# Kernel optimization log

Measured on AMD Instinct MI355X. Metric: run time of the kernel, lower is better.

The kernel has to match this reference:

```python
import jax, jax.numpy as jnp
import numpy as np

N_NODES, HID = 100000, 128
B, C, L, K = 64, 16, 256, 4


def setup_inputs() -> dict:
    key = jax.random.key(0)
    ks = jax.random.split(key, 6)
    s = 1.0 / np.sqrt(HID)
    return {
        "x": jax.random.normal(ks[0], (N_NODES, HID), dtype=jnp.float32),
        "leaf_idx": jax.random.randint(ks[1], (B, C, L), 0, N_NODES),
        "W_z": jax.random.normal(ks[2], (K, HID, HID), dtype=jnp.float32) * s,
        "W_z_final": jax.random.normal(ks[3], (HID, HID), dtype=jnp.float32) * s,
        "W_p": jax.random.normal(ks[4], (HID, HID), dtype=jnp.float32) * s,
        "W_p_final": jax.random.normal(ks[5], (HID, HID), dtype=jnp.float32) * s,
    }


def reference(x, leaf_idx, W_z, W_z_final, W_p, W_p_final):
    # Fixed ptree per sample: {'P': [{'Z': [L leaves]} x C]}
    k = W_z.shape[0]
    data = x[leaf_idx]                                   # [B,C,L,H] leaf gather (batch.x[subtree])
    # ---- z_layer_fn (vectorized over B,C) ----
    y = jnp.einsum("bclh,koh->kbclo", data, W_z)         # k bias-free Linears
    y = jax.vmap(lambda yk, s: jnp.roll(yk, -s, axis=2))(y, jnp.arange(k))  # roll along L by -idx
    z = jax.nn.elu(y.sum(axis=0))                        # sum over k, ELU  [B,C,L,H]
    z = jnp.einsum("bclh,oh->bclo", z, W_z_final).sum(axis=2)  # final linear, sum over L
    z = jax.nn.elu(z)                                    # [B,C,H]
    # ---- p_layer_fn over the C Z-children ----
    p = jnp.einsum("bch,oh->bco", z, W_p).sum(axis=1)    # p_layer, sum over children
    # apply_p_elu=False -> identity
    out = p @ W_p_final.T                                # [B,H]
    return out
```

## Files before the change

kernel.cpp:

```cpp
#include <hip/hip_runtime.h>
#include <hip/hip_bf16.h>

#define N_NODES 100000
#define HID 128
#define BB 64
#define CC 16
#define LL 256

typedef __bf16 b16x8 __attribute__((ext_vector_type(8)));
typedef float f32x4 __attribute__((ext_vector_type(4)));

__device__ __forceinline__ unsigned int bf16pair(float a, float b) {
  unsigned int ua = __float_as_uint(a), ub = __float_as_uint(b);
  ua = (ua + 0x7FFFu + ((ua >> 16) & 1u)) >> 16;
  ub = (ub + 0x7FFFu + ((ub >> 16) & 1u)) >> 16;
  return ua | (ub << 16);
}

__device__ __forceinline__ unsigned int cvtpk(float a, float b) {
  unsigned int r;
  asm("v_cvt_pk_bf16_f32 %0, %1, %2" : "=v"(r) : "v"(a), "v"(b));
  return r;
}

__device__ __forceinline__ float elu(float v) {
  return v > 0.f ? v : (__expf(v) - 1.f);
}

__global__ void k_prep(const float* __restrict__ Wz, uint4* __restrict__ wfrag) {
  const int u = blockIdx.x * 256 + threadIdx.x;
  const int lane = u & 63;
  const int ot = (u >> 6) & 7;
  const int ks = (u >> 9) & 3;
  const int kk = u >> 11;
  const int o = ot * 16 + (lane & 15);
  const int h0 = kk * 32 + (lane >> 4) * 8;
  const float4* src = (const float4*)(Wz + ((size_t)(ks * HID + o) * HID + h0));
  float4 f0 = src[0], f1 = src[1];
  uint4 pk;
  pk.x = bf16pair(f0.x, f0.y);
  pk.y = bf16pair(f0.z, f0.w);
  pk.z = bf16pair(f1.x, f1.y);
  pk.w = bf16pair(f1.z, f1.w);
  wfrag[u] = pk;
}

__global__ __launch_bounds__(512, 4) void k_main(
    const float* __restrict__ x, const int* __restrict__ leaf_idx,
    const uint4* __restrict__ wfrag, float* __restrict__ zsum) {
  extern __shared__ char smem[];
  char* sA = smem;
  uint4* sW = (uint4*)(smem + 65536);

  const int tid = threadIdx.x;
  const int bc = blockIdx.x;
  const int lane = tid & 63;
  const int l15 = lane & 15;
  const int hi = lane >> 4;
  const int w = tid >> 6;
  const int wr = w >> 1;
  const int wc = w & 1;

  {
    const int r = tid >> 1, half = tid & 1;
    const int idx = leaf_idx[bc * LL + r];
    const float4* src = (const float4*)(x + (size_t)idx * HID + half * 64);
    const int swz = (r & 15) << 4;
    char* rowp = sA + r * 256;
#pragma unroll
    for (int j = 0; j < 8; ++j) {
      float4 f0 = src[2 * j];
      float4 f1 = src[2 * j + 1];
      uint4 pk;
      pk.x = cvtpk(f0.x, f0.y);
      pk.y = cvtpk(f0.z, f0.w);
      pk.z = cvtpk(f1.x, f1.y);
      pk.w = cvtpk(f1.z, f1.w);
      *(uint4*)(rowp + (((half * 128) + j * 16) ^ swz)) = pk;
    }
  }
  sW[tid] = wfrag[tid];
  sW[512 + tid] = wfrag[512 + tid];
  __syncthreads();

  f32x4 acc[4][4];
#pragma unroll
  for (int rt = 0; rt < 4; ++rt)
#pragma unroll
    for (int ot = 0; ot < 4; ++ot) acc[rt][ot] = (f32x4){0.f, 0.f, 0.f, 0.f};

  const int r0 = wr * 64;

#pragma unroll
  for (int c = 0; c < 16; ++c) {
    const int kk = c >> 2, ks = c & 3;
    uint4 pref;
    if (c < 14) pref = wfrag[(c + 2) * 512 + tid];

    const uint4* sWc = sW + (c & 1) * 512;
    const int cb = kk * 64 + hi * 16;
    uint4 af[4];
#pragma unroll
    for (int rt = 0; rt < 4; ++rt) {
      const int row = (r0 + rt * 16 + l15 + ks) & 255;
      af[rt] = *(const uint4*)(sA + row * 256 + (cb ^ ((row & 15) << 4)));
    }
    __builtin_amdgcn_s_setprio(1);
#pragma unroll
    for (int ot2 = 0; ot2 < 4; ++ot2) {
      const uint4 bw = sWc[(wc * 4 + ot2) * 64 + lane];
      const b16x8 bb = __builtin_bit_cast(b16x8, bw);
#pragma unroll
      for (int rt = 0; rt < 4; ++rt)
        acc[rt][ot2] = __builtin_amdgcn_mfma_f32_16x16x32_bf16(
            __builtin_bit_cast(b16x8, af[rt]), bb, acc[rt][ot2], 0, 0, 0);
    }
    __builtin_amdgcn_s_setprio(0);
    __syncthreads();
    if (c < 14) sW[(c & 1) * 512 + tid] = pref;
  }

  float colsum[4];
#pragma unroll
  for (int ot2 = 0; ot2 < 4; ++ot2) {
    float s = 0.f;
#pragma unroll
    for (int rt = 0; rt < 4; ++rt)
#pragma unroll
      for (int q = 0; q < 4; ++q) s += elu(acc[rt][ot2][q]);
    s += __shfl_xor(s, 16);
    s += __shfl_xor(s, 32);
    colsum[ot2] = s;
  }
  float* sRed = (float*)sA;
  if (lane < 16) {
#pragma unroll
    for (int ot2 = 0; ot2 < 4; ++ot2)
      sRed[w * 64 + ot2 * 16 + lane] = colsum[ot2];
  }
  __syncthreads();
  if (tid < 128) {
    const int wc2 = tid >> 6, lc = tid & 63;
    float s = 0.f;
#pragma unroll
    for (int wrr = 0; wrr < 4; ++wrr) s += sRed[(wrr * 2 + wc2) * 64 + lc];
    zsum[bc * 128 + tid] = s;
  }
}

__global__ __launch_bounds__(512) void k_tail(
    const float* __restrict__ zsum, const float* __restrict__ Wzf,
    const float* __restrict__ Wp, const float* __restrict__ Wpf,
    float* __restrict__ out) {
  __shared__ float sZ[CC * HID];
  __shared__ float sS[4][HID];
  __shared__ float sV[HID];
  __shared__ float sP[HID];
  const int tid = threadIdx.x, b = blockIdx.x;
#pragma unroll
  for (int j = 0; j < 4; ++j)
    sZ[tid + j * 512] = zsum[(size_t)b * (CC * HID) + tid + j * 512];
  __syncthreads();

  {
    const int o = tid & 127, g = tid >> 7;
    const float4* wr4 = (const float4*)(Wzf + o * HID);
    float d0 = 0.f, d1 = 0.f, d2 = 0.f, d3 = 0.f;
#pragma unroll
    for (int j = 0; j < 32; ++j) {
      const float4 wv = wr4[j];
      const float4 z0 = *(const float4*)(sZ + (g * 4 + 0) * HID + j * 4);
      const float4 z1 = *(const float4*)(sZ + (g * 4 + 1) * HID + j * 4);
      const float4 z2v = *(const float4*)(sZ + (g * 4 + 2) * HID + j * 4);
      const float4 z3 = *(const float4*)(sZ + (g * 4 + 3) * HID + j * 4);
      d0 += wv.x * z0.x + wv.y * z0.y + wv.z * z0.z + wv.w * z0.w;
      d1 += wv.x * z1.x + wv.y * z1.y + wv.z * z1.z + wv.w * z1.w;
      d2 += wv.x * z2v.x + wv.y * z2v.y + wv.z * z2v.z + wv.w * z2v.w;
      d3 += wv.x * z3.x + wv.y * z3.y + wv.z * z3.z + wv.w * z3.w;
    }
    sS[g][o] = elu(d0) + elu(d1) + elu(d2) + elu(d3);
  }
  __syncthreads();
  if (tid < HID) sV[tid] = sS[0][tid] + sS[1][tid] + sS[2][tid] + sS[3][tid];
  __syncthreads();

  {
    const int o2 = tid >> 2, sub = tid & 3;
    const float4* wp4 = (const float4*)(Wp + o2 * HID + sub * 32);
    const float4* v4 = (const float4*)(sV + sub * 32);
    float d0 = 0.f, d1 = 0.f;
#pragma unroll
    for (int j = 0; j < 8; j += 2) {
      float4 a0 = wp4[j], c0 = v4[j];
      float4 a1 = wp4[j + 1], c1 = v4[j + 1];
      d0 += a0.x * c0.x + a0.y * c0.y + a0.z * c0.z + a0.w * c0.w;
      d1 += a1.x * c1.x + a1.y * c1.y + a1.z * c1.z + a1.w * c1.w;
    }
    float d = d0 + d1;
    d += __shfl_xor(d, 1);
    d += __shfl_xor(d, 2);
    if (sub == 0) sP[o2] = d;
  }
  __syncthreads();

  {
    const int o2 = tid >> 2, sub = tid & 3;
    const float4* wp4 = (const float4*)(Wpf + o2 * HID + sub * 32);
    const float4* p4 = (const float4*)(sP + sub * 32);
    float d0 = 0.f, d1 = 0.f;
#pragma unroll
    for (int j = 0; j < 8; j += 2) {
      float4 a0 = wp4[j], c0 = p4[j];
      float4 a1 = wp4[j + 1], c1 = p4[j + 1];
      d0 += a0.x * c0.x + a0.y * c0.y + a0.z * c0.z + a0.w * c0.w;
      d1 += a1.x * c1.x + a1.y * c1.y + a1.z * c1.z + a1.w * c1.w;
    }
    float d = d0 + d1;
    d += __shfl_xor(d, 1);
    d += __shfl_xor(d, 2);
    if (sub == 0) out[b * HID + o2] = d;
  }
}

extern "C" void kernel_launch(void* const* d_in, const int* in_sizes, int n_in,
                              void* d_out, int out_size, void* d_ws, size_t ws_size,
                              hipStream_t stream) {
  const float* x = (const float*)d_in[0];
  const int* leaf = (const int*)d_in[1];
  const float* Wz = (const float*)d_in[2];
  const float* Wzf = (const float*)d_in[3];
  const float* Wp = (const float*)d_in[4];
  const float* Wpf = (const float*)d_in[5];
  float* out = (float*)d_out;

  uint4* wfrag = (uint4*)d_ws;
  float* zsum = (float*)((char*)d_ws + 131072);

  (void)hipFuncSetAttribute((const void*)k_main,
                            hipFuncAttributeMaxDynamicSharedMemorySize, 81920);

  k_prep<<<32, 256, 0, stream>>>(Wz, wfrag);
  k_main<<<1024, 512, 81920, stream>>>(x, leaf, wfrag, zsum);
  k_tail<<<64, 512, 0, stream>>>(zsum, Wzf, Wp, Wpf, out);
}
```

Baseline: 61.83 us.

## Split each (b,c) tile across two 256-thread blocks with halo rows and atomic reduction

```diff
diff --git a/kernel.cpp b/kernel.cpp
--- a/kernel.cpp
+++ b/kernel.cpp
@@ -45,15 +45,17 @@
   wfrag[u] = pk;
 }
 
-__global__ __launch_bounds__(512, 4) void k_main(
+__global__ __launch_bounds__(256, 3) void k_main(
     const float* __restrict__ x, const int* __restrict__ leaf_idx,
     const uint4* __restrict__ wfrag, float* __restrict__ zsum) {
   extern __shared__ char smem[];
   char* sA = smem;
-  uint4* sW = (uint4*)(smem + 65536);
+  uint4* sW = (uint4*)(smem + 33792);
 
   const int tid = threadIdx.x;
-  const int bc = blockIdx.x;
+  const int bh = blockIdx.x;
+  const int bc = bh >> 1;
+  const int hbase = (bh & 1) * 128;
   const int lane = tid & 63;
   const int l15 = lane & 15;
   const int hi = lane >> 4;
@@ -62,11 +64,12 @@
   const int wc = w & 1;
 
   {
-    const int r = tid >> 1, half = tid & 1;
-    const int idx = leaf_idx[bc * LL + r];
-    const float4* src = (const float4*)(x + (size_t)idx * HID + half * 64);
-    const int swz = (r & 15) << 4;
-    char* rowp = sA + r * 256;
+    const int rl = tid >> 1, hc = tid & 1;
+    const int gr = (hbase + rl) & 255;
+    const int idx = leaf_idx[bc * LL + gr];
+    const float4* src = (const float4*)(x + (size_t)idx * HID + hc * 64);
+    const int swz = (rl & 15) << 4;
+    char* rowp = sA + rl * 256;
 #pragma unroll
     for (int j = 0; j < 8; ++j) {
       float4 f0 = src[2 * j];
@@ -76,11 +79,33 @@
       pk.y = cvtpk(f0.z, f0.w);
       pk.z = cvtpk(f1.x, f1.y);
       pk.w = cvtpk(f1.z, f1.w);
-      *(uint4*)(rowp + (((half * 128) + j * 16) ^ swz)) = pk;
-    }
-  }
-  sW[tid] = wfrag[tid];
-  sW[512 + tid] = wfrag[512 + tid];
+      *(uint4*)(rowp + (((hc * 128) + j * 16) ^ swz)) = pk;
+    }
+  }
+  if (tid < 6) {
+    const int rl = 128 + (tid >> 1), hc = tid & 1;
+    const int gr = (hbase + rl) & 255;
+    const int idx = leaf_idx[bc * LL + gr];
+    const float4* src = (const float4*)(x + (size_t)idx * HID + hc * 64);
+    const int swz = (rl & 15) << 4;
+    char* rowp = sA + rl * 256;
+#pragma unroll
+    for (int j = 0; j < 8; ++j) {
+      float4 f0 = src[2 * j];
+      float4 f1 = src[2 * j + 1];
+      uint4 pk;
+      pk.x = cvtpk(f0.x, f0.y);
+      pk.y = cvtpk(f0.z, f0.w);
+      pk.z = cvtpk(f1.x, f1.y);
+      pk.w = cvtpk(f1.z, f1.w);
+      *(uint4*)(rowp + (((hc * 128) + j * 16) ^ swz)) = pk;
+    }
+  }
+#pragma unroll
+  for (int i = 0; i < 2; ++i) {
+    sW[tid + i * 256] = wfrag[tid + i * 256];
+    sW[512 + tid + i * 256] = wfrag[512 + tid + i * 256];
+  }
   __syncthreads();
 
   f32x4 acc[4][4];
@@ -94,16 +119,19 @@
 #pragma unroll
   for (int c = 0; c < 16; ++c) {
     const int kk = c >> 2, ks = c & 3;
-    uint4 pref;
-    if (c < 14) pref = wfrag[(c + 2) * 512 + tid];
+    uint4 pref0, pref1;
+    if (c < 14) {
+      pref0 = wfrag[(c + 2) * 512 + tid];
+      pref1 = wfrag[(c + 2) * 512 + tid + 256];
+    }
 
     const uint4* sWc = sW + (c & 1) * 512;
     const int cb = kk * 64 + hi * 16;
     uint4 af[4];
 #pragma unroll
     for (int rt = 0; rt < 4; ++rt) {
-      const int row = (r0 + rt * 16 + l15 + ks) & 255;
-      af[rt] = *(const uint4*)(sA + row * 256 + (cb ^ ((row & 15) << 4)));
+      const int rr = r0 + rt * 16 + l15 + ks;
+      af[rt] = *(const uint4*)(sA + rr * 256 + (cb ^ ((rr & 15) << 4)));
     }
     __builtin_amdgcn_s_setprio(1);
 #pragma unroll
@@ -117,7 +145,10 @@
     }
     __builtin_amdgcn_s_setprio(0);
     __syncthreads();
-    if (c < 14) sW[(c & 1) * 512 + tid] = pref;
+    if (c < 14) {
+      sW[(c & 1) * 512 + tid] = pref0;
+      sW[(c & 1) * 512 + tid + 256] = pref1;
+    }
   }
 
   float colsum[4];
@@ -141,10 +172,8 @@
   __syncthreads();
   if (tid < 128) {
     const int wc2 = tid >> 6, lc = tid & 63;
-    float s = 0.f;
-#pragma unroll
-    for (int wrr = 0; wrr < 4; ++wrr) s += sRed[(wrr * 2 + wc2) * 64 + lc];
-    zsum[bc * 128 + tid] = s;
+    const float s = sRed[(0 * 2 + wc2) * 64 + lc] + sRed[(1 * 2 + wc2) * 64 + lc];
+    atomicAdd(&zsum[bc * 128 + tid], s);
   }
 }
 
@@ -178,10 +207,11 @@
       d2 += wv.x * z2v.x + wv.y * z2v.y + wv.z * z2v.z + wv.w * z2v.w;
       d3 += wv.x * z3.x + wv.y * z3.y + wv.z * z3.z + wv.w * z3.w;
     }
-    sS[g][o] = elu(d0) + elu(d1) + elu(d2) + elu(d3);
-  }
-  __syncthreads();
-  if (tid < HID) sV[tid] = sS[0][tid] + sS[1][tid] + sS[2][tid] + sS[3][tid];
+    sS[g][tid & 127] = elu(d0) + elu(d1) + elu(d2) + elu(d3);
+  }
+  __syncthreads();
+  if (tid < HID)
+    sV[tid] = sS[0][tid] + sS[1][tid] + sS[2][tid] + sS[3][tid];
   __syncthreads();
 
   {
@@ -237,9 +267,10 @@
   float* zsum = (float*)((char*)d_ws + 131072);
 
   (void)hipFuncSetAttribute((const void*)k_main,
-                            hipFuncAttributeMaxDynamicSharedMemorySize, 81920);
-
+                            hipFuncAttributeMaxDynamicSharedMemorySize, 50176);
+
+  (void)hipMemsetAsync(zsum, 0, 1024 * HID * sizeof(float), stream);
   k_prep<<<32, 256, 0, stream>>>(Wz, wfrag);
-  k_main<<<1024, 512, 81920, stream>>>(x, leaf, wfrag, zsum);
+  k_main<<<2048, 256, 50176, stream>>>(x, leaf, wfrag, zsum);
   k_tail<<<64, 512, 0, stream>>>(zsum, Wzf, Wp, Wpf, out);
 }
```

Result: slower. 71.18 us (+15.1%).
